# Kernel tuning notes

Measured on AMD Instinct MI355X. Metric: run time of the kernel, lower is better.

## Reference

```python
import jax, jax.numpy as jnp
import numpy as np

VOCAB = 32000
D = 1024        # d_model
E = 8           # n_experts
TOPK = 2        # routes per token
HOPS = 2        # n_hops (routers)
F = 2048        # expert hidden dim
T = 2048        # tokens
CAP_FACTOR = 1.25


def setup_inputs() -> dict:
    key = jax.random.key(0)
    k0, k1, k2, k3, k4 = jax.random.split(key, 5)
    ids_t = jax.random.randint(k0, (T,), 0, VOCAB)
    embed_w = jax.random.normal(k1, (VOCAB, D), jnp.float32) * 0.02
    router_w = jax.random.normal(k2, (HOPS, D, E), jnp.float32) * (1.0 / np.sqrt(D))
    w1 = jax.random.normal(k3, (E, D, F), jnp.float32) * (1.0 / np.sqrt(D))
    w2 = jax.random.normal(k4, (E, F, D), jnp.float32) * (1.0 / np.sqrt(F))
    ln_w = jnp.ones((D,), jnp.float32)
    return {"ids_t": ids_t, "embed_w": embed_w, "router_w": router_w,
            "w1": w1, "w2": w2, "ln_w": ln_w}


def _rmsnorm(x, w, eps=1e-6):
    return x * jax.lax.rsqrt(jnp.mean(x * x, axis=-1, keepdims=True) + eps) * w


def _topk_mask(logits_te, k):
    # boolean [T,E] mask of top-k experts per token
    Tn = logits_te.shape[0]
    _, idx = jax.lax.top_k(logits_te, k)                       # [T,k]
    mask = jnp.zeros(logits_te.shape, dtype=bool)
    return mask.at[jnp.arange(Tn)[:, None], idx].set(True)


def reference(ids_t, embed_w, router_w, w1, w2, ln_w):
    Tn = ids_t.shape[0]
    En = w1.shape[0]
    capacity = int(CAP_FACTOR * TOPK * Tn / En)                # static per-expert capacity

    h = embed_w[ids_t]                                         # [T,D] embedding lookup
    for hop in range(router_w.shape[0]):
        # --- router (TopKRouter): logits, full softmax probs, top-k mask ---
        logits_te = h @ router_w[hop]                          # [T,E]
        probs_te = jax.nn.softmax(logits_te, axis=-1)          # [T,E]
        mask_te = _topk_mask(logits_te, TOPK)                  # [T,E]
        # --- capacity limiting: keep first `capacity` routed tokens per expert ---
        rank_te = jnp.cumsum(mask_te.astype(jnp.int32), axis=0)
        kept_te = mask_te & (rank_te <= capacity)              # [T,E]
        # --- dense expert application (GELU MLP per expert) ---
        hid_etf = jnp.einsum('td,edf->etf', h, w1)             # [E,T,F]
        out_etd = jnp.einsum('etf,efd->etd', jax.nn.gelu(hid_etf), w2)  # [E,T,D]
        # --- rho-weighted residual combine ---
        kept_weight_te = jnp.where(kept_te, probs_te, 0.0)     # [T,E]
        combined_td = jnp.einsum('te,etd->td', kept_weight_te, out_etd)
        rho_t1 = kept_weight_te.sum(axis=-1, keepdims=True)    # [T,1]
        h = h + combined_td - rho_t1 * h

    h = _rmsnorm(h, ln_w)
    return h @ embed_w.T                                       # [T,vocab] tied projection
```

## Files before the change

kernel.cpp:

```cpp
#include <hip/hip_runtime.h>
#include <cstdint>

#define TK 2048
#define DM 1024
#define NE 8
#define NF 2048
#define NV 32000
#define CAP 640

typedef short bf16x8 __attribute__((ext_vector_type(8)));
typedef float floatx4 __attribute__((ext_vector_type(4)));

__device__ __forceinline__ unsigned short f2bf(float x){
  unsigned u = __float_as_uint(x);
  u += 0x7FFFu + ((u >> 16) & 1u);
  return (unsigned short)(u >> 16);
}
__device__ __forceinline__ float bf2f(unsigned short h){
  return __uint_as_float(((unsigned)h) << 16);
}
__device__ __forceinline__ float gelu_tanh(float x){
  float x3 = x*x*x;
  return 0.5f*x*(1.0f + tanhf(0.7978845608028654f*(x + 0.044715f*x3)));
}

__global__ void k_convert_bf16(const float* __restrict__ in, unsigned short* __restrict__ out, long n4){
  long i = (long)blockIdx.x*blockDim.x + threadIdx.x;
  if (i >= n4) return;
  float4 v = ((const float4*)in)[i];
  ushort4 o;
  o.x = f2bf(v.x); o.y = f2bf(v.y); o.z = f2bf(v.z); o.w = f2bf(v.w);
  ((ushort4*)out)[i] = o;
}

__global__ void k_transpose_split(const float* __restrict__ in, unsigned short* __restrict__ hi,
                                  unsigned short* __restrict__ lo, int R, int C){
  __shared__ float tile[32][33];
  const int b = blockIdx.z;
  const float* src = in + (long)b*R*C;
  const int c0 = blockIdx.x*32, r0 = blockIdx.y*32;
  const int tx = threadIdx.x, ty = threadIdx.y;
#pragma unroll
  for (int j=0;j<4;j++){
    int rr = ty + j*8;
    tile[rr][tx] = src[(long)(r0+rr)*C + (c0+tx)];
  }
  __syncthreads();
  unsigned short* dh = hi + (long)b*R*C;
  unsigned short* dl = lo + (long)b*R*C;
#pragma unroll
  for (int j=0;j<4;j++){
    int cc = ty + j*8;
    float v = tile[tx][cc];
    long o = (long)(c0+cc)*R + (r0+tx);
    unsigned short h_ = f2bf(v);
    dh[o] = h_;
    dl[o] = f2bf(v - bf2f(h_));
  }
}

__global__ void k_gather(const int* __restrict__ ids, const float* __restrict__ embed,
                         float* __restrict__ h, unsigned short* __restrict__ h_hi,
                         unsigned short* __restrict__ h_lo){
  const int t = blockIdx.x, tid = threadIdx.x;
  const int id = ids[t];
  float4 v = ((const float4*)(embed + (long)id*DM))[tid];
  ((float4*)(h + (long)t*DM))[tid] = v;
  ushort4 hh, ll;
  hh.x = f2bf(v.x); ll.x = f2bf(v.x - bf2f(hh.x));
  hh.y = f2bf(v.y); ll.y = f2bf(v.y - bf2f(hh.y));
  hh.z = f2bf(v.z); ll.z = f2bf(v.z - bf2f(hh.z));
  hh.w = f2bf(v.w); ll.w = f2bf(v.w - bf2f(hh.w));
  ((ushort4*)(h_hi + (long)t*DM))[tid] = hh;
  ((ushort4*)(h_lo + (long)t*DM))[tid] = ll;
}

__global__ void k_router(const float* __restrict__ h, const float* __restrict__ rw,
                         int* __restrict__ topk_e, float* __restrict__ topk_p,
                         int* __restrict__ tok_slot){
  const int t = blockIdx.x, lane = threadIdx.x;
  float acc[NE];
#pragma unroll
  for (int e=0;e<NE;e++) acc[e]=0.f;
  for (int i=0;i<DM/64;i++){
    int d = i*64 + lane;
    float hv = h[(long)t*DM + d];
    float4 r0 = ((const float4*)(rw + (long)d*NE))[0];
    float4 r1 = ((const float4*)(rw + (long)d*NE))[1];
    acc[0]+=hv*r0.x; acc[1]+=hv*r0.y; acc[2]+=hv*r0.z; acc[3]+=hv*r0.w;
    acc[4]+=hv*r1.x; acc[5]+=hv*r1.y; acc[6]+=hv*r1.z; acc[7]+=hv*r1.w;
  }
#pragma unroll
  for (int e=0;e<NE;e++){
#pragma unroll
    for (int off=32; off>=1; off>>=1) acc[e] += __shfl_xor(acc[e], off, 64);
  }
  if (lane==0){
    int e1=-1; float v1=-1e30f;
    for (int e=0;e<NE;e++) if (acc[e] > v1){ v1=acc[e]; e1=e; }
    int e2=-1; float v2=-1e30f;
    for (int e=0;e<NE;e++) if (e!=e1 && acc[e] > v2){ v2=acc[e]; e2=e; }
    float s=0.f;
    for (int e=0;e<NE;e++) s += expf(acc[e]-v1);
    topk_e[2*t]   = e1;  topk_e[2*t+1] = e2;
    topk_p[2*t]   = 1.0f/s;
    topk_p[2*t+1] = expf(v2-v1)/s;
    tok_slot[2*t] = -1;  tok_slot[2*t+1] = -1;
  }
}

__global__ void k_capacity(const int* __restrict__ topk_e, int* __restrict__ slot_token,
                           int* __restrict__ tok_slot){
  const int e = threadIdx.x >> 6, lane = threadIdx.x & 63;
  int running = 0;
  for (int base=0; base<TK; base+=64){
    int t = base + lane;
    int ea = topk_e[2*t], eb = topk_e[2*t+1];
    bool m = (ea==e) || (eb==e);
    unsigned long long bm = __ballot(m);
    int pre = __popcll(bm & (~0ull >> (63-lane)));
    if (m){
      int rank = running + pre;
      if (rank <= CAP){
        int slot = rank - 1;
        slot_token[e*CAP + slot] = t;
        int j = (ea==e) ? 0 : 1;
        tok_slot[2*t+j] = e*CAP + slot;
      }
    }
    running += __popcll(bm);
  }
  int total = running < CAP ? running : CAP;
  for (int s = total + lane; s < CAP; s += 64) slot_token[e*CAP+s] = -1;
}

template<bool SPLIT, bool GATHER, int EPI>
__global__ __launch_bounds__(256) void k_gemm(
    const unsigned short* __restrict__ Ahi, const unsigned short* __restrict__ Alo,
    const unsigned short* __restrict__ Bhi, const unsigned short* __restrict__ Blo,
    const int* __restrict__ rows,
    float* __restrict__ Cf, unsigned short* __restrict__ Chi, unsigned short* __restrict__ Clo,
    int K, int lda, int ldb, int ldc,
    long sA, long sB, long sC)
{
  constexpr int LDSW = 40;
  __shared__ unsigned short As_hi[128*LDSW];
  __shared__ unsigned short Bs_hi[128*LDSW];
  __shared__ unsigned short As_lo[SPLIT ? 128*LDSW : 64];
  __shared__ unsigned short Bs_lo[SPLIT ? 128*LDSW : 64];

  const int bm = blockIdx.x, bn = blockIdx.y, bz = blockIdx.z;
  const int tid = threadIdx.x;
  const int wid = tid>>6, lane = tid&63;
  const int wm = wid>>1, wn = wid&1;
  const int quad = lane>>4, l16 = lane&15;
  const int r = tid>>1, ccol = (tid&1)*16;

  const unsigned short* Abh = Ahi + (long)bz*sA;
  const unsigned short* Abl = SPLIT ? (Alo + (long)bz*sA) : Ahi;
  const unsigned short* Bbh = Bhi + (long)bz*sB;
  const unsigned short* Bbl = SPLIT ? (Blo + (long)bz*sB) : Bhi;

  long arow; bool avalid;
  if constexpr (GATHER){
    int t = rows[bz*CAP + bm*128 + r];
    avalid = (t >= 0); arow = avalid ? t : 0;
  } else { avalid = true; arow = (long)bm*128 + r; }
  const long aoff = arow*(long)lda + ccol;
  const long boff = ((long)bn*128 + r)*(long)ldb + ccol;

  uint4 ra0, ra1, rb0, rb1, ra0l, ra1l, rb0l, rb1l;
  const uint4 zz = make_uint4(0,0,0,0);

  auto stage_load = [&](int k0){
    if (avalid){
      ra0 = *(const uint4*)(Abh + aoff + k0);
      ra1 = *(const uint4*)(Abh + aoff + k0 + 8);
      if constexpr (SPLIT){
        ra0l = *(const uint4*)(Abl + aoff + k0);
        ra1l = *(const uint4*)(Abl + aoff + k0 + 8);
      }
    } else {
      ra0 = zz; ra1 = zz;
      if constexpr (SPLIT){ ra0l = zz; ra1l = zz; }
    }
    rb0 = *(const uint4*)(Bbh + boff + k0);
    rb1 = *(const uint4*)(Bbh + boff + k0 + 8);
    if constexpr (SPLIT){
      rb0l = *(const uint4*)(Bbl + boff + k0);
      rb1l = *(const uint4*)(Bbl + boff + k0 + 8);
    }
  };
  auto stage_store = [&](){
    *(uint4*)&As_hi[r*LDSW + ccol]     = ra0;
    *(uint4*)&As_hi[r*LDSW + ccol + 8] = ra1;
    *(uint4*)&Bs_hi[r*LDSW + ccol]     = rb0;
    *(uint4*)&Bs_hi[r*LDSW + ccol + 8] = rb1;
    if constexpr (SPLIT){
      *(uint4*)&As_lo[r*LDSW + ccol]     = ra0l;
      *(uint4*)&As_lo[r*LDSW + ccol + 8] = ra1l;
      *(uint4*)&Bs_lo[r*LDSW + ccol]     = rb0l;
      *(uint4*)&Bs_lo[r*LDSW + ccol + 8] = rb1l;
    }
  };

  floatx4 acc[4][4] = {};
  const int KT = K >> 5;
  stage_load(0);
  for (int kt=0; kt<KT; ++kt){
    __syncthreads();
    stage_store();
    __syncthreads();
    if (kt+1 < KT) stage_load((kt+1) << 5);

    bf16x8 ah[4], bh[4];
#pragma unroll
    for (int i=0;i<4;i++){
      ah[i] = *(const bf16x8*)&As_hi[(wm*64 + i*16 + l16)*LDSW + quad*8];
      bh[i] = *(const bf16x8*)&Bs_hi[(wn*64 + i*16 + l16)*LDSW + quad*8];
    }
#pragma unroll
    for (int mt=0;mt<4;mt++)
#pragma unroll
      for (int nt=0;nt<4;nt++)
        acc[mt][nt] = __builtin_amdgcn_mfma_f32_16x16x32_bf16(ah[mt], bh[nt], acc[mt][nt], 0,0,0);
    if constexpr (SPLIT){
      bf16x8 al[4], bl[4];
#pragma unroll
      for (int i=0;i<4;i++){
        al[i] = *(const bf16x8*)&As_lo[(wm*64 + i*16 + l16)*LDSW + quad*8];
        bl[i] = *(const bf16x8*)&Bs_lo[(wn*64 + i*16 + l16)*LDSW + quad*8];
      }
#pragma unroll
      for (int mt=0;mt<4;mt++)
#pragma unroll
        for (int nt=0;nt<4;nt++){
          acc[mt][nt] = __builtin_amdgcn_mfma_f32_16x16x32_bf16(ah[mt], bl[nt], acc[mt][nt], 0,0,0);
          acc[mt][nt] = __builtin_amdgcn_mfma_f32_16x16x32_bf16(al[mt], bh[nt], acc[mt][nt], 0,0,0);
        }
    }
  }

  if constexpr (EPI == 0){
    float* Cb = Cf + (long)bz*sC;
#pragma unroll
    for (int mt=0;mt<4;mt++)
#pragma unroll
      for (int nt=0;nt<4;nt++)
#pragma unroll
        for (int i=0;i<4;i++){
          int gr = bm*128 + wm*64 + mt*16 + quad*4 + i;
          int gc = bn*128 + wn*64 + nt*16 + l16;
          Cb[(long)gr*ldc + gc] = acc[mt][nt][i];
        }
  } else {
    unsigned short* Ch = Chi + (long)bz*sC;
    unsigned short* Cl = nullptr;
    if constexpr (SPLIT) Cl = Clo + (long)bz*sC;
#pragma unroll
    for (int mt=0;mt<4;mt++)
#pragma unroll
      for (int nt=0;nt<4;nt++)
#pragma unroll
        for (int i=0;i<4;i++){
          int gr = bm*128 + wm*64 + mt*16 + quad*4 + i;
          int gc = bn*128 + wn*64 + nt*16 + l16;
          float g = gelu_tanh(acc[mt][nt][i]);
          unsigned short hh = f2bf(g);
          long o = (long)gr*ldc + gc;
          Ch[o] = hh;
          if constexpr (SPLIT) Cl[o] = f2bf(g - bf2f(hh));
        }
  }
}

__global__ void k_combine(float* __restrict__ h, unsigned short* __restrict__ h_hi,
                          const float* __restrict__ out_e,
                          const int* __restrict__ tok_slot, const float* __restrict__ topk_p){
  const int t = blockIdx.x, tid = threadIdx.x;
  const int s0 = tok_slot[2*t], s1 = tok_slot[2*t+1];
  const float w0 = (s0>=0) ? topk_p[2*t]   : 0.f;
  const float w1 = (s1>=0) ? topk_p[2*t+1] : 0.f;
  const float sc = 1.f - w0 - w1;
#pragma unroll
  for (int i=0;i<4;i++){
    int d = i*256 + tid;
    float v = sc * h[(long)t*DM + d];
    if (s0>=0) v += w0 * out_e[(long)s0*DM + d];
    if (s1>=0) v += w1 * out_e[(long)s1*DM + d];
    h[(long)t*DM + d] = v;
    h_hi[(long)t*DM + d] = f2bf(v);
  }
}

__global__ void k_rmsnorm(const float* __restrict__ h, const float* __restrict__ lnw,
                          unsigned short* __restrict__ h_hi){
  const int t = blockIdx.x, tid = threadIdx.x;
  const int wid = tid>>6, lane = tid&63;
  float vals[4];
  float ss = 0.f;
#pragma unroll
  for (int i=0;i<4;i++){ vals[i] = h[(long)t*DM + i*256 + tid]; ss += vals[i]*vals[i]; }
#pragma unroll
  for (int off=32; off>=1; off>>=1) ss += __shfl_xor(ss, off, 64);
  __shared__ float red[4];
  __shared__ float scale_s;
  if (lane==0) red[wid] = ss;
  __syncthreads();
  if (tid==0) scale_s = 1.0f / sqrtf((red[0]+red[1]+red[2]+red[3])/(float)DM + 1e-6f);
  __syncthreads();
  float scale = scale_s;
#pragma unroll
  for (int i=0;i<4;i++){
    int d = i*256 + tid;
    h_hi[(long)t*DM + d] = f2bf(vals[i]*scale*lnw[d]);
  }
}

extern "C" void kernel_launch(void* const* d_in, const int* in_sizes, int n_in,
                              void* d_out, int out_size, void* d_ws, size_t ws_size,
                              hipStream_t stream){
  const int*   ids   = (const int*)d_in[0];
  const float* embed = (const float*)d_in[1];
  const float* rw    = (const float*)d_in[2];
  const float* w1    = (const float*)d_in[3];
  const float* w2    = (const float*)d_in[4];
  const float* lnw   = (const float*)d_in[5];

  char* ws = (char*)d_ws;
  auto alloc = [&](size_t b)->char*{ char* p = ws; ws += (b + 255) & ~(size_t)255; return p; };
  unsigned short* embed_bf = (unsigned short*)alloc((size_t)NV*DM*2);
  float*          h        = (float*)alloc((size_t)TK*DM*4);
  unsigned short* h_hi     = (unsigned short*)alloc((size_t)TK*DM*2);
  unsigned short* h_lo     = (unsigned short*)alloc((size_t)TK*DM*2);
  int*   topk_e   = (int*)alloc(TK*2*4);
  float* topk_p   = (float*)alloc(TK*2*4);
  int*   tok_slot = (int*)alloc(TK*2*4);
  int*   slot_tok = (int*)alloc(NE*CAP*4);

  char* od = (char*)d_out;
  auto alloc2 = [&](size_t b)->char*{ char* p = od; od += (b + 255) & ~(size_t)255; return p; };
  unsigned short* w1t_hi = (unsigned short*)alloc2((size_t)NE*DM*NF*2);
  unsigned short* w1t_lo = (unsigned short*)alloc2((size_t)NE*DM*NF*2);
  unsigned short* w2t_hi = (unsigned short*)alloc2((size_t)NE*DM*NF*2);
  unsigned short* w2t_lo = (unsigned short*)alloc2((size_t)NE*DM*NF*2);
  unsigned short* act_hi = (unsigned short*)alloc2((size_t)NE*CAP*NF*2);
  unsigned short* act_lo = (unsigned short*)alloc2((size_t)NE*CAP*NF*2);
  float*          out_e  = (float*)alloc2((size_t)NE*CAP*DM*4);

  dim3 tb32(32,8,1);
  k_transpose_split<<<dim3(NF/32, DM/32, NE), tb32, 0, stream>>>(w1, w1t_hi, w1t_lo, DM, NF);
  k_transpose_split<<<dim3(DM/32, NF/32, NE), tb32, 0, stream>>>(w2, w2t_hi, w2t_lo, NF, DM);
  k_convert_bf16<<<(int)(((long)NV*DM/4 + 255)/256), 256, 0, stream>>>(embed, embed_bf, (long)NV*DM/4);
  k_gather<<<TK, 256, 0, stream>>>(ids, embed, h, h_hi, h_lo);

  for (int hop=0; hop<2; ++hop){
    k_router<<<TK, 64, 0, stream>>>(h, rw + (long)hop*DM*NE, topk_e, topk_p, tok_slot);
    k_capacity<<<1, 512, 0, stream>>>(topk_e, slot_tok, tok_slot);
    if (hop == 0){
      k_gemm<true,true,1><<<dim3(CAP/128, NF/128, NE), 256, 0, stream>>>(
        h_hi, h_lo, w1t_hi, w1t_lo, slot_tok, nullptr, act_hi, act_lo,
        DM, DM, DM, NF, 0L, (long)NF*DM, (long)CAP*NF);
      k_gemm<true,false,0><<<dim3(CAP/128, DM/128, NE), 256, 0, stream>>>(
        act_hi, act_lo, w2t_hi, w2t_lo, nullptr, out_e, nullptr, nullptr,
        NF, NF, NF, DM, (long)CAP*NF, (long)DM*NF, (long)CAP*DM);
    } else {
      k_gemm<false,true,1><<<dim3(CAP/128, NF/128, NE), 256, 0, stream>>>(
        h_hi, nullptr, w1t_hi, nullptr, slot_tok, nullptr, act_hi, nullptr,
        DM, DM, DM, NF, 0L, (long)NF*DM, (long)CAP*NF);
      k_gemm<false,false,0><<<dim3(CAP/128, DM/128, NE), 256, 0, stream>>>(
        act_hi, nullptr, w2t_hi, nullptr, nullptr, out_e, nullptr, nullptr,
        NF, NF, NF, DM, (long)CAP*NF, (long)DM*NF, (long)CAP*DM);
    }
    k_combine<<<TK, 256, 0, stream>>>(h, h_hi, out_e, tok_slot, topk_p);
  }

  k_rmsnorm<<<TK, 256, 0, stream>>>(h, lnw, h_hi);
  k_gemm<false,false,0><<<dim3(TK/128, NV/128, 1), 256, 0, stream>>>(
    h_hi, nullptr, embed_bf, nullptr, nullptr, (float*)d_out, nullptr, nullptr,
    DM, DM, DM, NV, 0L, 0L, 0L);
}
```

Before: 1.024 ms.

## Replace final vocab projection GEMM with 256x256-tile pipelined direct-to-LDS kernel

Adds a new 512-thread GEMM kernel with 256x256 output tiles that loads A and B directly from global memory into swizzled LDS via global_load_lds. It double-buffers K-steps and interleaves LDS fragment loads, async stages and MFMA quads with barriers and setprio. It is used only for the final tied-embedding projection (2048x32000x1024), replacing the generic 128x128 GEMM. The aim is more operand reuse per tile and overlap of global loads with MFMA work, at the cost of 128KB dynamic LDS per block, lower occupancy and a tightly hand-scheduled wait-count pipeline that is fragile if K or the shapes change.

```diff
diff --git a/kernel.cpp b/kernel.cpp
--- a/kernel.cpp
+++ b/kernel.cpp
@@ -274,6 +274,137 @@
   }
 }
 
+__device__ __forceinline__ void gld_lds16(const void* g, void* l){
+  __builtin_amdgcn_global_load_lds((const __attribute__((address_space(1))) void*)g,
+                                   (__attribute__((address_space(3))) void*)l, 16, 0, 0);
+}
+
+__global__ __launch_bounds__(512, 2) void k_gemm256(
+    const unsigned short* __restrict__ A, const unsigned short* __restrict__ B,
+    float* __restrict__ C, int K, int ldc, int nbm)
+{
+  extern __shared__ unsigned short lds[];
+  const int bid = blockIdx.x;
+  const int bm = bid % nbm, bn = bid / nbm;
+  const int tid = threadIdx.x;
+  const int wid = tid >> 6, lane = tid & 63;
+  const int wm = wid >> 2, wn = wid & 3;
+  const int l16 = lane & 15, quad = lane >> 4;
+
+  const int srow = wid*8 + (lane>>3);
+  const int scol = ((lane&7) ^ (lane>>3)) << 3;
+
+  const unsigned short* Agl = A + ((long)bm*256 + srow)*(long)K + scol;
+  const unsigned short* Bgl = B + ((long)bn*256 + srow)*(long)K + scol;
+  const long rK64  = (long)64*K;
+  const long rK128 = (long)128*K;
+
+  floatx4 acc[8][4] = {};
+  bf16x8 a[4][2], b[4][2];
+
+#define STAGE_A(bufi, half, kt) do{ \
+    const unsigned short* g_ = Agl + (half)*rK128 + (long)(kt)*64; \
+    unsigned short* l_ = lds + ((bufi)*2+(half))*8192 + wid*512; \
+    gld_lds16(g_, l_); gld_lds16(g_ + rK64, l_ + 4096); }while(0)
+#define STAGE_B(bufi, half, kt) do{ \
+    const unsigned short* g_ = Bgl + (half)*rK128 + (long)(kt)*64; \
+    unsigned short* l_ = lds + 32768 + ((bufi)*2+(half))*8192 + wid*512; \
+    gld_lds16(g_, l_); gld_lds16(g_ + rK64, l_ + 4096); }while(0)
+
+#define LDF(slot, rh, kk) \
+    (*(const bf16x8*)((const char*)(slot) + (((((rh)<<7) + (kk)*64 + ((quad)<<4))) ^ (((rh)&7)<<4))))
+
+#define LOAD_A4(bufi, mq) do{ \
+    const unsigned short* s_ = lds + ((bufi)*2 + wm)*8192; \
+    _Pragma("unroll") for (int m_=0;m_<4;m_++){ \
+      int rh_ = ((mq)*4+m_)*16 + l16; \
+      a[m_][0] = LDF(s_, rh_, 0); a[m_][1] = LDF(s_, rh_, 1); } }while(0)
+#define LOAD_B2(bufi, nh) do{ \
+    const unsigned short* s_ = lds + 32768 + ((bufi)*2 + (wn>>1))*8192; \
+    _Pragma("unroll") for (int n_=0;n_<2;n_++){ \
+      int rh_ = (wn&1)*64 + ((nh)*2+n_)*16 + l16; \
+      b[(nh)*2+n_][0] = LDF(s_, rh_, 0); b[(nh)*2+n_][1] = LDF(s_, rh_, 1); } }while(0)
+
+#define PH_SYNC() do{ \
+    __builtin_amdgcn_s_barrier(); \
+    asm volatile("s_waitcnt lgkmcnt(0)" ::: "memory"); \
+    __builtin_amdgcn_sched_barrier(0); }while(0)
+
+#define MFMA_QUAD(mq, nq) do{ \
+    __builtin_amdgcn_s_setprio(1); \
+    _Pragma("unroll") for (int m_=0;m_<4;m_++) \
+    _Pragma("unroll") for (int n_=0;n_<2;n_++) \
+    _Pragma("unroll") for (int kk_=0;kk_<2;kk_++) \
+      acc[(mq)*4+m_][(nq)*2+n_] = __builtin_amdgcn_mfma_f32_16x16x32_bf16( \
+        a[m_][kk_], b[(nq)*2+n_][kk_], acc[(mq)*4+m_][(nq)*2+n_], 0,0,0); \
+    __builtin_amdgcn_s_setprio(0); \
+    __builtin_amdgcn_s_barrier(); }while(0)
+
+  STAGE_A(0,0,0); STAGE_A(0,1,0);
+  STAGE_B(0,0,0); STAGE_B(0,1,0);
+  STAGE_B(1,0,1); STAGE_B(1,1,1);
+  asm volatile("s_waitcnt vmcnt(4)" ::: "memory");
+  __builtin_amdgcn_s_barrier();
+
+  const int NI = K >> 7;
+#pragma unroll 1
+  for (int i = 0; i < NI-1; ++i){
+    const int tb = 2*i+1, t2 = 2*i+2, t3 = 2*i+3;
+    LOAD_A4(0,0); LOAD_B2(0,0); STAGE_A(1,0,tb);
+    PH_SYNC(); MFMA_QUAD(0,0);
+    LOAD_B2(0,1); STAGE_A(1,1,tb);
+    PH_SYNC(); MFMA_QUAD(0,1);
+    LOAD_A4(0,1); STAGE_B(0,0,t2);
+    PH_SYNC(); MFMA_QUAD(1,0);
+    STAGE_B(0,1,t2);
+    asm volatile("s_waitcnt vmcnt(4)" ::: "memory");
+    PH_SYNC(); MFMA_QUAD(1,1);
+    LOAD_A4(1,0); LOAD_B2(1,0); STAGE_A(0,0,t2);
+    PH_SYNC(); MFMA_QUAD(0,0);
+    LOAD_B2(1,1); STAGE_A(0,1,t2);
+    PH_SYNC(); MFMA_QUAD(0,1);
+    LOAD_A4(1,1); STAGE_B(1,0,t3);
+    PH_SYNC(); MFMA_QUAD(1,0);
+    STAGE_B(1,1,t3);
+    asm volatile("s_waitcnt vmcnt(4)" ::: "memory");
+    PH_SYNC(); MFMA_QUAD(1,1);
+  }
+  {
+    const int tb = 2*NI-1;
+    LOAD_A4(0,0); LOAD_B2(0,0); STAGE_A(1,0,tb);
+    PH_SYNC(); MFMA_QUAD(0,0);
+    LOAD_B2(0,1); STAGE_A(1,1,tb);
+    PH_SYNC(); MFMA_QUAD(0,1);
+    LOAD_A4(0,1);
+    PH_SYNC(); MFMA_QUAD(1,0);
+    asm volatile("s_waitcnt vmcnt(0)" ::: "memory");
+    PH_SYNC(); MFMA_QUAD(1,1);
+    LOAD_A4(1,0); LOAD_B2(1,0);
+    PH_SYNC(); MFMA_QUAD(0,0);
+    LOAD_B2(1,1);
+    PH_SYNC(); MFMA_QUAD(0,1);
+    LOAD_A4(1,1);
+    PH_SYNC(); MFMA_QUAD(1,0);
+    PH_SYNC(); MFMA_QUAD(1,1);
+  }
+#undef STAGE_A
+#undef STAGE_B
+#undef LDF
+#undef LOAD_A4
+#undef LOAD_B2
+#undef PH_SYNC
+#undef MFMA_QUAD
+
+  float* Cp = C + ((long)bm*256 + wm*128 + quad*4)*(long)ldc + (long)bn*256 + wn*64 + l16;
+#pragma unroll
+  for (int m_=0;m_<8;m_++)
+#pragma unroll
+    for (int n_=0;n_<4;n_++)
+#pragma unroll
+      for (int i_=0;i_<4;i_++)
+        Cp[(long)(m_*16 + i_)*ldc + n_*16] = acc[m_][n_][i_];
+}
+
 __global__ void k_combine(float* __restrict__ h, unsigned short* __restrict__ h_hi,
                           const float* __restrict__ out_e,
                           const int* __restrict__ tok_slot, const float* __restrict__ topk_p){
@@ -326,6 +457,13 @@
   const float* w1    = (const float*)d_in[3];
   const float* w2    = (const float*)d_in[4];
   const float* lnw   = (const float*)d_in[5];
+
+  static bool attr_done = false;
+  if (!attr_done){
+    hipFuncSetAttribute(reinterpret_cast<const void*>(k_gemm256),
+                        hipFuncAttributeMaxDynamicSharedMemorySize, 131072);
+    attr_done = true;
+  }
 
   char* ws = (char*)d_ws;
   auto alloc = [&](size_t b)->char*{ char* p = ws; ws += (b + 255) & ~(size_t)255; return p; };
@@ -376,7 +514,6 @@
   }
 
   k_rmsnorm<<<TK, 256, 0, stream>>>(h, lnw, h_hi);
-  k_gemm<false,false,0><<<dim3(TK/128, NV/128, 1), 256, 0, stream>>>(
-    h_hi, nullptr, embed_bf, nullptr, nullptr, (float*)d_out, nullptr, nullptr,
-    DM, DM, DM, NV, 0L, 0L, 0L);
-}
+  k_gemm256<<<dim3(8*(NV/256)), 512, 131072, stream>>>(
+    h_hi, embed_bf, (float*)d_out, DM, NV, 8);
+}
```

Measured after the change: 1.144 ms. 11.7% more time.

## Load GEMM tiles directly into LDS with global_load_lds

Applied to the files above, without the earlier changes.

Operand tiles in the GEMM now go straight from global memory to shared memory through the direct-to-LDS load builtin. This removes the register staging and the separate LDS store instructions. The LDS row stride drops from 40 to 32 elements (no padding) so each wave's rows are contiguous, as the direct load layout requires. The change also drops the register prefetch of the next k-tile, so loads no longer overlap compute. Unpadded rows may cause LDS bank conflicts on the MFMA fragment reads, and invalid gathered rows now read row 0 instead of zeros.

```diff
diff --git a/kernel.cpp b/kernel.cpp
--- a/kernel.cpp
+++ b/kernel.cpp
@@ -22,6 +22,10 @@
 __device__ __forceinline__ float gelu_tanh(float x){
   float x3 = x*x*x;
   return 0.5f*x*(1.0f + tanhf(0.7978845608028654f*(x + 0.044715f*x3)));
+}
+__device__ __forceinline__ void gld_lds16(const unsigned short* g, unsigned short* l){
+  __builtin_amdgcn_global_load_lds((const __attribute__((address_space(1))) void*)g,
+                                   (__attribute__((address_space(3))) void*)l, 16, 0, 0);
 }
 
 __global__ void k_convert_bf16(const float* __restrict__ in, unsigned short* __restrict__ out, long n4){
@@ -143,7 +147,7 @@
     int K, int lda, int ldb, int ldc,
     long sA, long sB, long sC)
 {
-  constexpr int LDSW = 40;
+  constexpr int LDSW = 32;
   __shared__ unsigned short As_hi[128*LDSW];
   __shared__ unsigned short Bs_hi[128*LDSW];
   __shared__ unsigned short As_lo[SPLIT ? 128*LDSW : 64];
@@ -154,64 +158,56 @@
   const int wid = tid>>6, lane = tid&63;
   const int wm = wid>>1, wn = wid&1;
   const int quad = lane>>4, l16 = lane&15;
-  const int r = tid>>1, ccol = (tid&1)*16;
 
   const unsigned short* Abh = Ahi + (long)bz*sA;
   const unsigned short* Abl = SPLIT ? (Alo + (long)bz*sA) : Ahi;
   const unsigned short* Bbh = Bhi + (long)bz*sB;
   const unsigned short* Bbl = SPLIT ? (Blo + (long)bz*sB) : Bhi;
 
-  long arow; bool avalid;
+  const int srow0 = wid*32 + (lane>>2);
+  const int srow1 = srow0 + 16;
+  const int scol  = (lane&3)*8;
+
+  long arow0, arow1;
   if constexpr (GATHER){
-    int t = rows[bz*CAP + bm*128 + r];
-    avalid = (t >= 0); arow = avalid ? t : 0;
-  } else { avalid = true; arow = (long)bm*128 + r; }
-  const long aoff = arow*(long)lda + ccol;
-  const long boff = ((long)bn*128 + r)*(long)ldb + ccol;
-
-  uint4 ra0, ra1, rb0, rb1, ra0l, ra1l, rb0l, rb1l;
-  const uint4 zz = make_uint4(0,0,0,0);
-
-  auto stage_load = [&](int k0){
-    if (avalid){
-      ra0 = *(const uint4*)(Abh + aoff + k0);
-      ra1 = *(const uint4*)(Abh + aoff + k0 + 8);
-      if constexpr (SPLIT){
-        ra0l = *(const uint4*)(Abl + aoff + k0);
-        ra1l = *(const uint4*)(Abl + aoff + k0 + 8);
-      }
-    } else {
-      ra0 = zz; ra1 = zz;
-      if constexpr (SPLIT){ ra0l = zz; ra1l = zz; }
-    }
-    rb0 = *(const uint4*)(Bbh + boff + k0);
-    rb1 = *(const uint4*)(Bbh + boff + k0 + 8);
-    if constexpr (SPLIT){
-      rb0l = *(const uint4*)(Bbl + boff + k0);
-      rb1l = *(const uint4*)(Bbl + boff + k0 + 8);
-    }
-  };
-  auto stage_store = [&](){
-    *(uint4*)&As_hi[r*LDSW + ccol]     = ra0;
-    *(uint4*)&As_hi[r*LDSW + ccol + 8] = ra1;
-    *(uint4*)&Bs_hi[r*LDSW + ccol]     = rb0;
-    *(uint4*)&Bs_hi[r*LDSW + ccol + 8] = rb1;
-    if constexpr (SPLIT){
-      *(uint4*)&As_lo[r*LDSW + ccol]     = ra0l;
-      *(uint4*)&As_lo[r*LDSW + ccol + 8] = ra1l;
-      *(uint4*)&Bs_lo[r*LDSW + ccol]     = rb0l;
-      *(uint4*)&Bs_lo[r*LDSW + ccol + 8] = rb1l;
-    }
-  };
+    int t0 = rows[bz*CAP + bm*128 + srow0];
+    int t1 = rows[bz*CAP + bm*128 + srow1];
+    arow0 = (t0 >= 0) ? t0 : 0;
+    arow1 = (t1 >= 0) ? t1 : 0;
+  } else {
+    arow0 = (long)bm*128 + srow0;
+    arow1 = (long)bm*128 + srow1;
+  }
+  const unsigned short* Ah0 = Abh + arow0*(long)lda + scol;
+  const unsigned short* Ah1 = Abh + arow1*(long)lda + scol;
+  const unsigned short* Al0 = Abl + arow0*(long)lda + scol;
+  const unsigned short* Al1 = Abl + arow1*(long)lda + scol;
+  const unsigned short* Bh0 = Bbh + ((long)bn*128 + srow0)*(long)ldb + scol;
+  const unsigned short* Bh1 = Bbh + ((long)bn*128 + srow1)*(long)ldb + scol;
+  const unsigned short* Bl0 = Bbl + ((long)bn*128 + srow0)*(long)ldb + scol;
+  const unsigned short* Bl1 = Bbl + ((long)bn*128 + srow1)*(long)ldb + scol;
+
+  unsigned short* AsD = As_hi + wid*1024;
+  unsigned short* BsD = Bs_hi + wid*1024;
+  unsigned short* AsDl = As_lo + wid*1024;
+  unsigned short* BsDl = Bs_lo + wid*1024;
 
   floatx4 acc[4][4] = {};
   const int KT = K >> 5;
-  stage_load(0);
   for (int kt=0; kt<KT; ++kt){
+    const int k0 = kt << 5;
     __syncthreads();
-    stage_store();
+    gld_lds16(Ah0 + k0, AsD);
+    gld_lds16(Ah1 + k0, AsD + 512);
+    gld_lds16(Bh0 + k0, BsD);
+    gld_lds16(Bh1 + k0, BsD + 512);
+    if constexpr (SPLIT){
+      gld_lds16(Al0 + k0, AsDl);
+      gld_lds16(Al1 + k0, AsDl + 512);
+      gld_lds16(Bl0 + k0, BsDl);
+      gld_lds16(Bl1 + k0, BsDl + 512);
+    }
     __syncthreads();
-    if (kt+1 < KT) stage_load((kt+1) << 5);
 
     bf16x8 ah[4], bh[4];
 #pragma unroll
```

Result: slower. 1.049 ms (+2.4%).
